# Performance work log

Measured on AMD Instinct MI355X. Metric: run time of the kernel, lower is better.

Reference implementation:

```python
import jax, jax.numpy as jnp
import numpy as np

WH, WW, WD = 4, 4, 4
NUM_HEADS = 12


def _relative_coords():
    # (3, N) flattened coords of the 3D window, N = WH*WW*WD
    g = jnp.stack(jnp.meshgrid(jnp.arange(WH), jnp.arange(WW), jnp.arange(WD), indexing='ij'), axis=0)
    flat = g.reshape(3, -1)
    rel = flat[:, :, None] - flat[:, None, :]          # (3, N, N)
    return jnp.transpose(rel, (1, 2, 0)).astype(jnp.float32)  # (N, N, 3)


def setup_inputs() -> dict:
    key = jax.random.key(0)
    ks = jax.random.split(key, 9)
    B_, N, C = 2048, WH * WW * WD, 384
    s = lambda fan: 1.0 / np.sqrt(fan)
    return {
        'x': jax.random.normal(ks[0], (B_, N, C), jnp.float32),
        'qkv_w': jax.random.normal(ks[1], (C, 3 * C), jnp.float32) * s(C),
        'qkv_b': jax.random.normal(ks[2], (3 * C,), jnp.float32) * 0.02,
        'proj_w': jax.random.normal(ks[3], (C, C), jnp.float32) * s(C),
        'proj_b': jax.random.normal(ks[4], (C,), jnp.float32) * 0.02,
        'mlp_w1': jax.random.normal(ks[5], (3, 64), jnp.float32) * s(3),
        'mlp_b1': jax.random.normal(ks[6], (64,), jnp.float32) * 0.02,
        'mlp_w2': jax.random.normal(ks[7], (64, NUM_HEADS), jnp.float32) * s(64),
        'mlp_b2': jax.random.normal(ks[8], (NUM_HEADS,), jnp.float32) * 0.02,
    }


def reference(x, qkv_w, qkv_b, proj_w, proj_b, mlp_w1, mlp_b1, mlp_w2, mlp_b2):
    B_, N, C = x.shape
    H = NUM_HEADS
    hd = C // H
    scale = hd ** -0.5

    qkv = (x @ qkv_w + qkv_b).reshape(B_, N, 3, H, hd)
    q, k, v = qkv[:, :, 0], qkv[:, :, 1], qkv[:, :, 2]   # (B_, N, H, hd)

    # MLP-based relative position bias: (N, N, 3) -> (H, N, N)
    rel = _relative_coords()
    bias = jax.nn.relu(rel @ mlp_w1 + mlp_b1) @ mlp_w2 + mlp_b2  # (N, N, H)
    bias = jnp.transpose(bias, (2, 0, 1))                        # (H, N, N)

    attn = jnp.einsum('bnhd,bmhd->bhnm', q, k) * scale + bias[None]
    attn = jax.nn.softmax(attn, axis=-1)

    out = jnp.einsum('bhnm,bmhd->bnhd', attn, v).reshape(B_, N, C)
    return out @ proj_w + proj_b
```

## Files before the change

kernel.cpp:

```cpp
#include <hip/hip_runtime.h>
#include <stdint.h>

#define NTOK 64
#define CDIM 384
#define NH   12
#define HD   32
#define SCALE 0.17677669529663687f

typedef __attribute__((ext_vector_type(8))) short short8;
typedef __attribute__((ext_vector_type(4))) float floatx4;

__device__ __forceinline__ unsigned short f2bf(float f) {
    union { float f; unsigned u; } v; v.f = f;
    unsigned r = (v.u + 0x7fffu + ((v.u >> 16) & 1u)) >> 16;
    return (unsigned short)r;
}

__global__ void prep_weights(const float* __restrict__ qkv_w,
                             const float* __restrict__ proj_w,
                             unsigned short* __restrict__ qkv_wt,
                             unsigned short* __restrict__ proj_wt) {
    int i = blockIdx.x * blockDim.x + threadIdx.x;
    const int nq = 1152 * 384;
    const int np = 384 * 384;
    if (i < nq) {
        int r = i / 384, c = i - r * 384;
        qkv_wt[i] = f2bf(qkv_w[c * 1152 + r]);
    } else if (i < nq + np) {
        int o = i - nq;
        int r = o / 384, c = o - r * 384;
        proj_wt[o] = f2bf(proj_w[c * 384 + r]);
    }
}

__global__ void prep_bias(const float* __restrict__ w1, const float* __restrict__ b1,
                          const float* __restrict__ w2, const float* __restrict__ b2,
                          float* __restrict__ bt) {
    int t = blockIdx.x * blockDim.x + threadIdx.x;
    int i = t >> 6, j = t & 63;
    float r0 = (float)((i >> 4) - (j >> 4));
    float r1 = (float)(((i >> 2) & 3) - ((j >> 2) & 3));
    float r2 = (float)((i & 3) - (j & 3));
    float acc[NH];
#pragma unroll
    for (int h = 0; h < NH; ++h) acc[h] = b2[h];
    for (int u = 0; u < 64; ++u) {
        float hv = r0 * w1[u] + r1 * w1[64 + u] + r2 * w1[128 + u] + b1[u];
        hv = fmaxf(hv, 0.f);
#pragma unroll
        for (int h = 0; h < NH; ++h) acc[h] += hv * w2[u * NH + h];
    }
    for (int h = 0; h < NH; ++h) bt[(h << 12) + (i << 6) + j] = acc[h];
}

#define XP  392
#define QKP 40
#define VTP 72
#define PBP 72

__launch_bounds__(256, 1)
__global__ void win_attn(const float* __restrict__ x,
                         const unsigned short* __restrict__ qkv_wt,
                         const float* __restrict__ qkv_b,
                         const unsigned short* __restrict__ proj_wt,
                         const float* __restrict__ proj_b,
                         const float* __restrict__ bt,
                         float* __restrict__ out) {
    __shared__ unsigned short xs[64 * XP];
    __shared__ unsigned short ao[64 * XP];
    __shared__ unsigned short qls[2][64 * QKP];
    __shared__ unsigned short kls[2][64 * QKP];
    __shared__ unsigned short vts[2][32 * VTP];
    __shared__ unsigned short pbs[2][64 * PBP];
    const int tid  = threadIdx.x;
    const int lane = tid & 63;
    const int w    = tid >> 6;
    const int l15  = lane & 15;
    const int quad = lane >> 4;
    const int b    = blockIdx.x;

    const float* xb = x + (size_t)b * (64 * 384);
    for (int it = 0; it < 24; ++it) {
        int idx = it * 256 + tid;
        int row = idx / 96;
        int c4  = idx - row * 96;
        const float4 v = *reinterpret_cast<const float4*>(xb + row * 384 + c4 * 4);
        uint2 pk;
        pk.x = (unsigned)f2bf(v.x) | ((unsigned)f2bf(v.y) << 16);
        pk.y = (unsigned)f2bf(v.z) | ((unsigned)f2bf(v.w) << 16);
        *reinterpret_cast<uint2*>(&xs[row * XP + c4 * 4]) = pk;
    }
    __syncthreads();

    const int hh = w >> 1;
    const int d2 = w & 1;
    float rs[2][4];
    const floatx4 zf4 = {0.f, 0.f, 0.f, 0.f};

#pragma unroll 1
    for (int hp = 0; hp < 6; ++hp) {
        floatx4 acc[3][4];
#pragma unroll
        for (int j = 0; j < 3; ++j)
#pragma unroll
            for (int m = 0; m < 4; ++m) acc[j][m] = zf4;

        int colbase[3];
#pragma unroll
        for (int j = 0; j < 3; ++j)
            colbase[j] = j * 384 + (2 * hp + hh) * 32 + d2 * 16;

#pragma unroll
        for (int kk = 0; kk < 12; ++kk) {
            short8 a[4];
#pragma unroll
            for (int m = 0; m < 4; ++m)
                a[m] = *reinterpret_cast<const short8*>(
                    &xs[(16 * m + l15) * XP + kk * 32 + quad * 8]);
#pragma unroll
            for (int j = 0; j < 3; ++j) {
                const short8 bf = *reinterpret_cast<const short8*>(
                    qkv_wt + (size_t)(colbase[j] + l15) * 384 + kk * 32 + quad * 8);
#pragma unroll
                for (int m = 0; m < 4; ++m)
                    acc[j][m] = __builtin_amdgcn_mfma_f32_16x16x32_bf16(a[m], bf, acc[j][m], 0, 0, 0);
            }
        }
#pragma unroll
        for (int j = 0; j < 3; ++j) {
            const float bc = qkv_b[colbase[j] + l15];
            if (j < 2) {
                unsigned short* dst = (j == 0) ? qls[hh] : kls[hh];
#pragma unroll
                for (int m = 0; m < 4; ++m)
#pragma unroll
                    for (int r = 0; r < 4; ++r) {
                        int tok = 16 * m + quad * 4 + r;
                        dst[tok * QKP + d2 * 16 + l15] = f2bf(acc[j][m][r] + bc);
                    }
            } else {
#pragma unroll
                for (int m = 0; m < 4; ++m) {
                    uint2 pk;
                    pk.x = (unsigned)f2bf(acc[2][m][0] + bc) | ((unsigned)f2bf(acc[2][m][1] + bc) << 16);
                    pk.y = (unsigned)f2bf(acc[2][m][2] + bc) | ((unsigned)f2bf(acc[2][m][3] + bc) << 16);
                    *reinterpret_cast<uint2*>(
                        &vts[hh][(d2 * 16 + l15) * VTP + 16 * m + quad * 4]) = pk;
                }
            }
        }
        __syncthreads();

#pragma unroll
        for (int hi = 0; hi < 2; ++hi) {
            const int h = 2 * hp + hi;
            const short8 aq = *reinterpret_cast<const short8*>(
                &qls[hi][(16 * w + l15) * QKP + quad * 8]);
            floatx4 s4[4];
#pragma unroll
            for (int c = 0; c < 4; ++c) {
                const short8 bk = *reinterpret_cast<const short8*>(
                    &kls[hi][(16 * c + l15) * QKP + quad * 8]);
                s4[c] = __builtin_amdgcn_mfma_f32_16x16x32_bf16(aq, bk, zf4, 0, 0, 0);
            }
            const float* bth = bt + ((size_t)h << 12);
#pragma unroll
            for (int r = 0; r < 4; ++r) {
                const int n = 16 * w + quad * 4 + r;
#pragma unroll
                for (int c = 0; c < 4; ++c)
                    s4[c][r] = s4[c][r] * SCALE + bth[(n << 6) + 16 * c + l15];
                float m0 = fmaxf(fmaxf(s4[0][r], s4[1][r]), fmaxf(s4[2][r], s4[3][r]));
#pragma unroll
                for (int sh = 1; sh < 16; sh <<= 1) m0 = fmaxf(m0, __shfl_xor(m0, sh, 16));
                float p0 = 0.f;
#pragma unroll
                for (int c = 0; c < 4; ++c) {
                    float p = __expf(s4[c][r] - m0);
                    s4[c][r] = p;
                    p0 += p;
                }
#pragma unroll
                for (int sh = 1; sh < 16; sh <<= 1) p0 += __shfl_xor(p0, sh, 16);
                rs[hi][r] = 1.f / p0;
#pragma unroll
                for (int c = 0; c < 4; ++c)
                    pbs[hi][n * PBP + 16 * c + l15] = f2bf(s4[c][r]);
            }
        }
        __syncthreads();

#pragma unroll
        for (int hi = 0; hi < 2; ++hi) {
            const int h = 2 * hp + hi;
            short8 ap[2];
#pragma unroll
            for (int kk = 0; kk < 2; ++kk)
                ap[kk] = *reinterpret_cast<const short8*>(
                    &pbs[hi][(16 * w + l15) * PBP + kk * 32 + quad * 8]);
#pragma unroll
            for (int t = 0; t < 2; ++t) {
                floatx4 oacc = zf4;
#pragma unroll
                for (int kk = 0; kk < 2; ++kk) {
                    const short8 bv = *reinterpret_cast<const short8*>(
                        &vts[hi][(16 * t + l15) * VTP + kk * 32 + quad * 8]);
                    oacc = __builtin_amdgcn_mfma_f32_16x16x32_bf16(ap[kk], bv, oacc, 0, 0, 0);
                }
#pragma unroll
                for (int r = 0; r < 4; ++r) {
                    int tok = 16 * w + quad * 4 + r;
                    ao[tok * XP + h * 32 + 16 * t + l15] = f2bf(oacc[r] * rs[hi][r]);
                }
            }
        }
        __syncthreads();
    }

    float* ob = out + (size_t)b * (64 * 384);
#pragma unroll 1
    for (int pass = 0; pass < 2; ++pass) {
        const int ntb = pass * 12 + w * 3;
        floatx4 acc2[3][4];
#pragma unroll
        for (int j = 0; j < 3; ++j)
#pragma unroll
            for (int m = 0; m < 4; ++m) acc2[j][m] = zf4;

#pragma unroll
        for (int kk = 0; kk < 12; ++kk) {
            short8 a2[4];
#pragma unroll
            for (int m = 0; m < 4; ++m)
                a2[m] = *reinterpret_cast<const short8*>(
                    &ao[(16 * m + l15) * XP + kk * 32 + quad * 8]);
#pragma unroll
            for (int j = 0; j < 3; ++j) {
                const short8 bf = *reinterpret_cast<const short8*>(
                    proj_wt + (size_t)((ntb + j) * 16 + l15) * 384 + kk * 32 + quad * 8);
#pragma unroll
                for (int m = 0; m < 4; ++m)
                    acc2[j][m] = __builtin_amdgcn_mfma_f32_16x16x32_bf16(a2[m], bf, acc2[j][m], 0, 0, 0);
            }
        }
#pragma unroll
        for (int j = 0; j < 3; ++j) {
            const int col = (ntb + j) * 16 + l15;
            const float pbias = proj_b[col];
#pragma unroll
            for (int m = 0; m < 4; ++m)
#pragma unroll
                for (int r = 0; r < 4; ++r)
                    ob[(16 * m + quad * 4 + r) * 384 + col] = acc2[j][m][r] + pbias;
        }
    }
}

extern "C" void kernel_launch(void* const* d_in, const int* in_sizes, int n_in,
                              void* d_out, int out_size, void* d_ws, size_t ws_size,
                              hipStream_t stream) {
    const float* x      = (const float*)d_in[0];
    const float* qkv_w  = (const float*)d_in[1];
    const float* qkv_b  = (const float*)d_in[2];
    const float* proj_w = (const float*)d_in[3];
    const float* proj_b = (const float*)d_in[4];
    const float* mlp_w1 = (const float*)d_in[5];
    const float* mlp_b1 = (const float*)d_in[6];
    const float* mlp_w2 = (const float*)d_in[7];
    const float* mlp_b2 = (const float*)d_in[8];
    float* out = (float*)d_out;

    unsigned short* qkv_wt  = (unsigned short*)d_ws;
    unsigned short* proj_wt = qkv_wt + 1152 * 384;
    float*          bt      = (float*)(proj_wt + 384 * 384);

    prep_weights<<<2304, 256, 0, stream>>>(qkv_w, proj_w, qkv_wt, proj_wt);
    prep_bias<<<16, 256, 0, stream>>>(mlp_w1, mlp_b1, mlp_w2, mlp_b2, bt);
    win_attn<<<2048, 256, 0, stream>>>(x, qkv_wt, qkv_b, proj_wt, proj_b, bt, out);
}
```

Before: 870.8 us.

## Fuse projection into head loop, keep x in registers, raise occupancy

The x tile now lives in registers as bf16 MFMA fragments instead of a large LDS buffer. Each wave computes Q/K/V for its own 16 tokens per head, which removes one LDS barrier stage. The output projection is accumulated per head pair inside the loop using a small LDS staging buffer, so the full 64x384 attention-output buffer is no longer needed. Together these cut LDS use enough to allow two blocks per CU. Weight prep switches to a tiled, coalesced transpose kernel. The cost is heavy register pressure from 24 persistent accumulators plus 12 A fragments, and repeated global weight loads from each wave.

```diff
diff --git a/kernel.cpp b/kernel.cpp
--- a/kernel.cpp
+++ b/kernel.cpp
@@ -1,10 +1,6 @@
 #include <hip/hip_runtime.h>
 #include <stdint.h>
 
-#define NTOK 64
-#define CDIM 384
-#define NH   12
-#define HD   32
 #define SCALE 0.17677669529663687f
 
 typedef __attribute__((ext_vector_type(8))) short short8;
@@ -16,49 +12,50 @@
     return (unsigned short)r;
 }
 
-__global__ void prep_weights(const float* __restrict__ qkv_w,
-                             const float* __restrict__ proj_w,
-                             unsigned short* __restrict__ qkv_wt,
-                             unsigned short* __restrict__ proj_wt) {
-    int i = blockIdx.x * blockDim.x + threadIdx.x;
-    const int nq = 1152 * 384;
-    const int np = 384 * 384;
-    if (i < nq) {
-        int r = i / 384, c = i - r * 384;
-        qkv_wt[i] = f2bf(qkv_w[c * 1152 + r]);
-    } else if (i < nq + np) {
-        int o = i - nq;
-        int r = o / 384, c = o - r * 384;
-        proj_wt[o] = f2bf(proj_w[c * 384 + r]);
+__global__ void transpose_bf16(const float* __restrict__ in, unsigned short* __restrict__ out,
+                               int R, int Cc) {
+    __shared__ float t[32][33];
+    const int tx = threadIdx.x & 31, ty = threadIdx.x >> 5;
+    const int c0 = blockIdx.x * 32, r0 = blockIdx.y * 32;
+#pragma unroll
+    for (int i = 0; i < 4; ++i) {
+        int r = ty + i * 8;
+        t[r][tx] = in[(size_t)(r0 + r) * Cc + c0 + tx];
+    }
+    __syncthreads();
+#pragma unroll
+    for (int i = 0; i < 4; ++i) {
+        int rr = ty + i * 8;
+        out[(size_t)(c0 + rr) * R + r0 + tx] = f2bf(t[tx][rr]);
     }
 }
 
 __global__ void prep_bias(const float* __restrict__ w1, const float* __restrict__ b1,
                           const float* __restrict__ w2, const float* __restrict__ b2,
                           float* __restrict__ bt) {
-    int t = blockIdx.x * blockDim.x + threadIdx.x;
+    int t = blockIdx.x * 64 + threadIdx.x;
     int i = t >> 6, j = t & 63;
     float r0 = (float)((i >> 4) - (j >> 4));
     float r1 = (float)(((i >> 2) & 3) - ((j >> 2) & 3));
     float r2 = (float)((i & 3) - (j & 3));
-    float acc[NH];
-#pragma unroll
-    for (int h = 0; h < NH; ++h) acc[h] = b2[h];
+    float acc[12];
+#pragma unroll
+    for (int h = 0; h < 12; ++h) acc[h] = b2[h];
     for (int u = 0; u < 64; ++u) {
         float hv = r0 * w1[u] + r1 * w1[64 + u] + r2 * w1[128 + u] + b1[u];
         hv = fmaxf(hv, 0.f);
 #pragma unroll
-        for (int h = 0; h < NH; ++h) acc[h] += hv * w2[u * NH + h];
-    }
-    for (int h = 0; h < NH; ++h) bt[(h << 12) + (i << 6) + j] = acc[h];
-}
-
-#define XP  392
+        for (int h = 0; h < 12; ++h) acc[h] += hv * w2[u * 12 + h];
+    }
+    for (int h = 0; h < 12; ++h) bt[(h << 12) + (i << 6) + j] = acc[h];
+}
+
 #define QKP 40
 #define VTP 72
 #define PBP 72
-
-__launch_bounds__(256, 1)
+#define AOP 72
+
+__launch_bounds__(256, 2)
 __global__ void win_attn(const float* __restrict__ x,
                          const unsigned short* __restrict__ qkv_wt,
                          const float* __restrict__ qkv_b,
@@ -66,87 +63,80 @@
                          const float* __restrict__ proj_b,
                          const float* __restrict__ bt,
                          float* __restrict__ out) {
-    __shared__ unsigned short xs[64 * XP];
-    __shared__ unsigned short ao[64 * XP];
     __shared__ unsigned short qls[2][64 * QKP];
     __shared__ unsigned short kls[2][64 * QKP];
     __shared__ unsigned short vts[2][32 * VTP];
-    __shared__ unsigned short pbs[2][64 * PBP];
+    __shared__ unsigned short pbs[64 * PBP];
+    __shared__ unsigned short aop[64 * AOP];
     const int tid  = threadIdx.x;
     const int lane = tid & 63;
     const int w    = tid >> 6;
     const int l15  = lane & 15;
     const int quad = lane >> 4;
     const int b    = blockIdx.x;
-
-    const float* xb = x + (size_t)b * (64 * 384);
-    for (int it = 0; it < 24; ++it) {
-        int idx = it * 256 + tid;
-        int row = idx / 96;
-        int c4  = idx - row * 96;
-        const float4 v = *reinterpret_cast<const float4*>(xb + row * 384 + c4 * 4);
-        uint2 pk;
-        pk.x = (unsigned)f2bf(v.x) | ((unsigned)f2bf(v.y) << 16);
-        pk.y = (unsigned)f2bf(v.z) | ((unsigned)f2bf(v.w) << 16);
-        *reinterpret_cast<uint2*>(&xs[row * XP + c4 * 4]) = pk;
-    }
-    __syncthreads();
-
-    const int hh = w >> 1;
-    const int d2 = w & 1;
-    float rs[2][4];
     const floatx4 zf4 = {0.f, 0.f, 0.f, 0.f};
+
+    const float* xr = x + ((size_t)b * 64 + 16 * w + l15) * 384 + quad * 8;
+    short8 af[12];
+#pragma unroll
+    for (int kk = 0; kk < 12; ++kk) {
+        const float4 u0 = *reinterpret_cast<const float4*>(xr + kk * 32);
+        const float4 u1 = *reinterpret_cast<const float4*>(xr + kk * 32 + 4);
+        short8 t;
+        t[0] = (short)f2bf(u0.x); t[1] = (short)f2bf(u0.y);
+        t[2] = (short)f2bf(u0.z); t[3] = (short)f2bf(u0.w);
+        t[4] = (short)f2bf(u1.x); t[5] = (short)f2bf(u1.y);
+        t[6] = (short)f2bf(u1.z); t[7] = (short)f2bf(u1.w);
+        af[kk] = t;
+    }
+
+    floatx4 acc2[6][4];
+#pragma unroll
+    for (int j = 0; j < 6; ++j)
+#pragma unroll
+        for (int m = 0; m < 4; ++m) acc2[j][m] = zf4;
 
 #pragma unroll 1
     for (int hp = 0; hp < 6; ++hp) {
-        floatx4 acc[3][4];
-#pragma unroll
-        for (int j = 0; j < 3; ++j)
-#pragma unroll
-            for (int m = 0; m < 4; ++m) acc[j][m] = zf4;
-
-        int colbase[3];
-#pragma unroll
-        for (int j = 0; j < 3; ++j)
-            colbase[j] = j * 384 + (2 * hp + hh) * 32 + d2 * 16;
-
-#pragma unroll
-        for (int kk = 0; kk < 12; ++kk) {
-            short8 a[4];
-#pragma unroll
-            for (int m = 0; m < 4; ++m)
-                a[m] = *reinterpret_cast<const short8*>(
-                    &xs[(16 * m + l15) * XP + kk * 32 + quad * 8]);
-#pragma unroll
-            for (int j = 0; j < 3; ++j) {
-                const short8 bf = *reinterpret_cast<const short8*>(
-                    qkv_wt + (size_t)(colbase[j] + l15) * 384 + kk * 32 + quad * 8);
-#pragma unroll
-                for (int m = 0; m < 4; ++m)
-                    acc[j][m] = __builtin_amdgcn_mfma_f32_16x16x32_bf16(a[m], bf, acc[j][m], 0, 0, 0);
-            }
-        }
-#pragma unroll
-        for (int j = 0; j < 3; ++j) {
-            const float bc = qkv_b[colbase[j] + l15];
-            if (j < 2) {
-                unsigned short* dst = (j == 0) ? qls[hh] : kls[hh];
-#pragma unroll
-                for (int m = 0; m < 4; ++m)
-#pragma unroll
-                    for (int r = 0; r < 4; ++r) {
-                        int tok = 16 * m + quad * 4 + r;
-                        dst[tok * QKP + d2 * 16 + l15] = f2bf(acc[j][m][r] + bc);
-                    }
-            } else {
-#pragma unroll
-                for (int m = 0; m < 4; ++m) {
-                    uint2 pk;
-                    pk.x = (unsigned)f2bf(acc[2][m][0] + bc) | ((unsigned)f2bf(acc[2][m][1] + bc) << 16);
-                    pk.y = (unsigned)f2bf(acc[2][m][2] + bc) | ((unsigned)f2bf(acc[2][m][3] + bc) << 16);
-                    *reinterpret_cast<uint2*>(
-                        &vts[hh][(d2 * 16 + l15) * VTP + 16 * m + quad * 4]) = pk;
+#pragma unroll
+        for (int hi = 0; hi < 2; ++hi) {
+            const int h = 2 * hp + hi;
+            floatx4 qa[2], ka[2], va[2];
+#pragma unroll
+            for (int t = 0; t < 2; ++t) { qa[t] = zf4; ka[t] = zf4; va[t] = zf4; }
+            const unsigned short* wb = qkv_wt + ((size_t)h * 32 + l15) * 384 + quad * 8;
+#pragma unroll
+            for (int kk = 0; kk < 12; ++kk) {
+                const short8 bq0 = *reinterpret_cast<const short8*>(wb + kk * 32);
+                const short8 bq1 = *reinterpret_cast<const short8*>(wb + 6144 + kk * 32);
+                const short8 bk0 = *reinterpret_cast<const short8*>(wb + 147456 + kk * 32);
+                const short8 bk1 = *reinterpret_cast<const short8*>(wb + 147456 + 6144 + kk * 32);
+                const short8 bv0 = *reinterpret_cast<const short8*>(wb + 294912 + kk * 32);
+                const short8 bv1 = *reinterpret_cast<const short8*>(wb + 294912 + 6144 + kk * 32);
+                qa[0] = __builtin_amdgcn_mfma_f32_16x16x32_bf16(af[kk], bq0, qa[0], 0, 0, 0);
+                qa[1] = __builtin_amdgcn_mfma_f32_16x16x32_bf16(af[kk], bq1, qa[1], 0, 0, 0);
+                ka[0] = __builtin_amdgcn_mfma_f32_16x16x32_bf16(af[kk], bk0, ka[0], 0, 0, 0);
+                ka[1] = __builtin_amdgcn_mfma_f32_16x16x32_bf16(af[kk], bk1, ka[1], 0, 0, 0);
+                va[0] = __builtin_amdgcn_mfma_f32_16x16x32_bf16(af[kk], bv0, va[0], 0, 0, 0);
+                va[1] = __builtin_amdgcn_mfma_f32_16x16x32_bf16(af[kk], bv1, va[1], 0, 0, 0);
+            }
+#pragma unroll
+            for (int t = 0; t < 2; ++t) {
+                const int col = h * 32 + t * 16 + l15;
+                const float bq = qkv_b[col];
+                const float bk = qkv_b[384 + col];
+                const float bv = qkv_b[768 + col];
+#pragma unroll
+                for (int r = 0; r < 4; ++r) {
+                    const int tok = 16 * w + 4 * quad + r;
+                    qls[hi][tok * QKP + t * 16 + l15] = f2bf(qa[t][r] + bq);
+                    kls[hi][tok * QKP + t * 16 + l15] = f2bf(ka[t][r] + bk);
                 }
+                uint2 pk;
+                pk.x = (unsigned)f2bf(va[t][0] + bv) | ((unsigned)f2bf(va[t][1] + bv) << 16);
+                pk.y = (unsigned)f2bf(va[t][2] + bv) | ((unsigned)f2bf(va[t][3] + bv) << 16);
+                *reinterpret_cast<uint2*>(
+                    &vts[hi][(t * 16 + l15) * VTP + 16 * w + 4 * quad]) = pk;
             }
         }
         __syncthreads();
@@ -164,9 +154,10 @@
                 s4[c] = __builtin_amdgcn_mfma_f32_16x16x32_bf16(aq, bk, zf4, 0, 0, 0);
             }
             const float* bth = bt + ((size_t)h << 12);
+            float rs[4];
 #pragma unroll
             for (int r = 0; r < 4; ++r) {
-                const int n = 16 * w + quad * 4 + r;
+                const int n = 16 * w + 4 * quad + r;
 #pragma unroll
                 for (int c = 0; c < 4; ++c)
                     s4[c][r] = s4[c][r] * SCALE + bth[(n << 6) + 16 * c + l15];
@@ -182,77 +173,64 @@
                 }
 #pragma unroll
                 for (int sh = 1; sh < 16; sh <<= 1) p0 += __shfl_xor(p0, sh, 16);
-                rs[hi][r] = 1.f / p0;
+                rs[r] = 1.f / p0;
 #pragma unroll
                 for (int c = 0; c < 4; ++c)
-                    pbs[hi][n * PBP + 16 * c + l15] = f2bf(s4[c][r]);
+                    pbs[n * PBP + 16 * c + l15] = f2bf(s4[c][r]);
+            }
+            __asm__ volatile("" ::: "memory");
+
+            const short8 ap0 = *reinterpret_cast<const short8*>(
+                &pbs[(16 * w + l15) * PBP + quad * 8]);
+            const short8 ap1 = *reinterpret_cast<const short8*>(
+                &pbs[(16 * w + l15) * PBP + 32 + quad * 8]);
+#pragma unroll
+            for (int t = 0; t < 2; ++t) {
+                floatx4 o = zf4;
+                const short8 bv0 = *reinterpret_cast<const short8*>(
+                    &vts[hi][(16 * t + l15) * VTP + quad * 8]);
+                const short8 bv1 = *reinterpret_cast<const short8*>(
+                    &vts[hi][(16 * t + l15) * VTP + 32 + quad * 8]);
+                o = __builtin_amdgcn_mfma_f32_16x16x32_bf16(ap0, bv0, o, 0, 0, 0);
+                o = __builtin_amdgcn_mfma_f32_16x16x32_bf16(ap1, bv1, o, 0, 0, 0);
+#pragma unroll
+                for (int r = 0; r < 4; ++r)
+                    aop[(16 * w + 4 * quad + r) * AOP + hi * 32 + 16 * t + l15] =
+                        f2bf(o[r] * rs[r]);
             }
         }
         __syncthreads();
 
-#pragma unroll
-        for (int hi = 0; hi < 2; ++hi) {
-            const int h = 2 * hp + hi;
-            short8 ap[2];
-#pragma unroll
-            for (int kk = 0; kk < 2; ++kk)
-                ap[kk] = *reinterpret_cast<const short8*>(
-                    &pbs[hi][(16 * w + l15) * PBP + kk * 32 + quad * 8]);
-#pragma unroll
-            for (int t = 0; t < 2; ++t) {
-                floatx4 oacc = zf4;
-#pragma unroll
-                for (int kk = 0; kk < 2; ++kk) {
-                    const short8 bv = *reinterpret_cast<const short8*>(
-                        &vts[hi][(16 * t + l15) * VTP + kk * 32 + quad * 8]);
-                    oacc = __builtin_amdgcn_mfma_f32_16x16x32_bf16(ap[kk], bv, oacc, 0, 0, 0);
-                }
-#pragma unroll
-                for (int r = 0; r < 4; ++r) {
-                    int tok = 16 * w + quad * 4 + r;
-                    ao[tok * XP + h * 32 + 16 * t + l15] = f2bf(oacc[r] * rs[hi][r]);
-                }
-            }
-        }
-        __syncthreads();
+        short8 ap2[4][2];
+#pragma unroll
+        for (int m = 0; m < 4; ++m) {
+            ap2[m][0] = *reinterpret_cast<const short8*>(&aop[(16 * m + l15) * AOP + quad * 8]);
+            ap2[m][1] = *reinterpret_cast<const short8*>(&aop[(16 * m + l15) * AOP + 32 + quad * 8]);
+        }
+#pragma unroll
+        for (int j = 0; j < 6; ++j) {
+            const unsigned short* pw =
+                proj_wt + ((size_t)(96 * w + 16 * j + l15)) * 384 + hp * 64 + quad * 8;
+            const short8 b0 = *reinterpret_cast<const short8*>(pw);
+            const short8 b1 = *reinterpret_cast<const short8*>(pw + 32);
+#pragma unroll
+            for (int m = 0; m < 4; ++m) {
+                acc2[j][m] = __builtin_amdgcn_mfma_f32_16x16x32_bf16(ap2[m][0], b0, acc2[j][m], 0, 0, 0);
+                acc2[j][m] = __builtin_amdgcn_mfma_f32_16x16x32_bf16(ap2[m][1], b1, acc2[j][m], 0, 0, 0);
+            }
+        }
     }
 
     float* ob = out + (size_t)b * (64 * 384);
-#pragma unroll 1
-    for (int pass = 0; pass < 2; ++pass) {
-        const int ntb = pass * 12 + w * 3;
-        floatx4 acc2[3][4];
-#pragma unroll
-        for (int j = 0; j < 3; ++j)
-#pragma unroll
-            for (int m = 0; m < 4; ++m) acc2[j][m] = zf4;
-
-#pragma unroll
-        for (int kk = 0; kk < 12; ++kk) {
-            short8 a2[4];
-#pragma unroll
-            for (int m = 0; m < 4; ++m)
-                a2[m] = *reinterpret_cast<const short8*>(
-                    &ao[(16 * m + l15) * XP + kk * 32 + quad * 8]);
-#pragma unroll
-            for (int j = 0; j < 3; ++j) {
-                const short8 bf = *reinterpret_cast<const short8*>(
-                    proj_wt + (size_t)((ntb + j) * 16 + l15) * 384 + kk * 32 + quad * 8);
-#pragma unroll
-                for (int m = 0; m < 4; ++m)
-                    acc2[j][m] = __builtin_amdgcn_mfma_f32_16x16x32_bf16(a2[m], bf, acc2[j][m], 0, 0, 0);
-            }
-        }
-#pragma unroll
-        for (int j = 0; j < 3; ++j) {
-            const int col = (ntb + j) * 16 + l15;
-            const float pbias = proj_b[col];
-#pragma unroll
-            for (int m = 0; m < 4; ++m)
-#pragma unroll
-                for (int r = 0; r < 4; ++r)
-                    ob[(16 * m + quad * 4 + r) * 384 + col] = acc2[j][m][r] + pbias;
-        }
+#pragma unroll
+    for (int j = 0; j < 6; ++j) {
+        const int col = 96 * w + 16 * j + l15;
+        const float pb = proj_b[col];
+#pragma unroll
+        for (int m = 0; m < 4; ++m)
+#pragma unroll
+            for (int r = 0; r < 4; ++r)
+                ob[(16 * m + 4 * quad + r) * 384 + col] = acc2[j][m][r] + pb;
     }
 }
 
@@ -274,7 +252,8 @@
     unsigned short* proj_wt = qkv_wt + 1152 * 384;
     float*          bt      = (float*)(proj_wt + 384 * 384);
 
-    prep_weights<<<2304, 256, 0, stream>>>(qkv_w, proj_w, qkv_wt, proj_wt);
-    prep_bias<<<16, 256, 0, stream>>>(mlp_w1, mlp_b1, mlp_w2, mlp_b2, bt);
+    transpose_bf16<<<dim3(36, 12), 256, 0, stream>>>(qkv_w, qkv_wt, 384, 1152);
+    transpose_bf16<<<dim3(12, 12), 256, 0, stream>>>(proj_w, proj_wt, 384, 384);
+    prep_bias<<<64, 64, 0, stream>>>(mlp_w1, mlp_b1, mlp_w2, mlp_b2, bt);
     win_attn<<<2048, 256, 0, stream>>>(x, qkv_wt, qkv_b, proj_wt, proj_b, bt, out);
 }
```

Measured after the change: 1.399 ms. +60.7%, slower.
